# Kernel optimization log

Hardware: AMD Instinct MI355X
Metric: run time of the kernel (lower is better)

Reference implementation:

```python
import jax, jax.numpy as jnp
import numpy as np

B, TAPE, OUT, FANIN = 64, 262144, 65536, 16


def setup_inputs() -> dict:
    key = jax.random.key(0)
    k1, k2, k3, k4 = jax.random.split(key, 4)
    tape = jax.random.normal(k1, (B, TAPE), dtype=jnp.float32)
    input_indices = jax.random.randint(k2, (OUT, FANIN), 0, TAPE, dtype=jnp.int64)
    # He initialization over fanin, zeroed at padding positions (index == 0)
    weights = jax.random.normal(k3, (OUT, FANIN), dtype=jnp.float32) * np.sqrt(2.0 / FANIN)
    weights = jnp.where(input_indices == 0, 0.0, weights)
    bias = jnp.zeros((OUT,), dtype=jnp.float32)
    output_indices = jnp.arange(OUT, dtype=jnp.int64)
    act_ids = jax.random.randint(k4, (OUT,), 0, 3, dtype=jnp.int64)  # 0=relu,1=sigmoid,2=tanh
    return {"tape": tape, "weights": weights, "bias": bias,
            "input_indices": input_indices, "output_indices": output_indices,
            "act_ids": act_ids}


def reference(tape, weights, bias, input_indices, output_indices, act_ids):
    # Gather neighbor values: [B, OUT, FANIN]
    gathered = jnp.take(tape, input_indices, axis=1)
    # Weighted sum over fanin + bias: [B, OUT]
    x = jnp.einsum('bof,of->bo', gathered, weights) + bias
    # Per-node activation dispatch (vectorized select over activation groups)
    x = jnp.where(act_ids == 0, jax.nn.relu(x),
                  jnp.where(act_ids == 1, jax.nn.sigmoid(x), jnp.tanh(x)))
    # Scatter results back into the tape
    tape = tape.at[:, output_indices].set(x)
    return tape
```

## Files before the change

kernel.cpp:

```cpp
#include <hip/hip_runtime.h>
#include <hip/hip_fp16.h>

#define B_SZ 64
#define TAPE_N 262144
#define OUT_N 65536
#define FANIN 16
#define XCDS 8

typedef _Float16 h16v __attribute__((ext_vector_type(16)));
typedef _Float16 h8v  __attribute__((ext_vector_type(8)));
typedef float    f4v  __attribute__((ext_vector_type(4)));

__global__ __launch_bounds__(256) void copy_transpose_kernel(
    const float* __restrict__ tape, float* __restrict__ out,
    _Float16* __restrict__ tape_T)
{
    __shared__ float lds[64][65];
    const int t0  = blockIdx.x * 64;
    const int tid = threadIdx.x;
    const bool do_copy = (t0 >= OUT_N);

    const int t4 = tid & 15;
    const int b0 = tid >> 4;
    #pragma unroll
    for (int r = 0; r < 4; ++r) {
        const int b = b0 + r * 16;
        const f4v v = __builtin_nontemporal_load(
            (const f4v*)(tape + (size_t)b * TAPE_N + t0 + t4 * 4));
        if (do_copy)
            __builtin_nontemporal_store(
                v, (f4v*)(out + (size_t)b * TAPE_N + t0 + t4 * 4));
        lds[t4 * 4 + 0][b] = v.x;
        lds[t4 * 4 + 1][b] = v.y;
        lds[t4 * 4 + 2][b] = v.z;
        lds[t4 * 4 + 3][b] = v.w;
    }
    __syncthreads();

    const int c    = tid & 7;
    const int trow = tid >> 3;
    #pragma unroll
    for (int p = 0; p < 2; ++p) {
        const int t = trow + p * 32;
        h8v v;
        #pragma unroll
        for (int j = 0; j < 8; ++j) v[j] = (_Float16)lds[t][c * 8 + j];
        *(h8v*)(tape_T + (size_t)(t0 + t) * 64 + c * 8) = v;
    }
}

__global__ __launch_bounds__(256) void neuron_t_kernel(
    const _Float16* __restrict__ tape_T,
    const float* __restrict__ weights,
    const float* __restrict__ bias,
    const int*   __restrict__ input_indices,
    const int*   __restrict__ output_indices,
    const int*   __restrict__ act_ids,
    float* __restrict__ out)
{
    __shared__ float so[64][65];
    __shared__ int   s_ok;

    const int tid = threadIdx.x;
    const int ol  = tid >> 2;
    const int o   = blockIdx.x * 64 + ol;
    const int bq  = tid & 3;

    if (tid == 0) s_ok = 1;

    const int4*   ip = (const int4*)(input_indices + (size_t)o * FANIN);
    const float4* wp = (const float4*)(weights      + (size_t)o * FANIN);
    const int4   I0 = ip[0], I1 = ip[1], I2 = ip[2], I3 = ip[3];
    const float4 W0 = wp[0], W1 = wp[1], W2 = wp[2], W3 = wp[3];
    const float bs  = bias[o];
    const int   act = act_ids[o];
    const int   od  = output_indices[o];

    const int   idx[16] = {I0.x, I0.y, I0.z, I0.w, I1.x, I1.y, I1.z, I1.w,
                           I2.x, I2.y, I2.z, I2.w, I3.x, I3.y, I3.z, I3.w};
    const float wv[16]  = {W0.x, W0.y, W0.z, W0.w, W1.x, W1.y, W1.z, W1.w,
                           W2.x, W2.y, W2.z, W2.w, W3.x, W3.y, W3.z, W3.w};

    float acc[16];
    #pragma unroll
    for (int k = 0; k < 16; ++k) acc[k] = bs;

    const _Float16* tb = tape_T + bq * 16;

    #pragma unroll
    for (int f = 0; f < FANIN; ++f) {
        const h16v v = *(const h16v*)(tb + (size_t)idx[f] * 64);
        const float w = wv[f];
        #pragma unroll
        for (int k = 0; k < 16; ++k) acc[k] += w * (float)v[k];
    }

    if (od != o) s_ok = 0;

    #pragma unroll
    for (int k = 0; k < 16; ++k) {
        const float x = acc[k];
        float z = (act == 1) ? 0.5f * x : x;
        z = fminf(fmaxf(z, -15.0f), 15.0f);
        const float e  = __expf(-2.0f * z);
        const float th = (1.0f - e) / (1.0f + e);
        const float y = (act == 0) ? fmaxf(x, 0.0f)
                       : (act == 1) ? 0.5f * (th + 1.0f)
                                    : th;
        so[bq * 16 + k][ol] = y;
    }
    __syncthreads();

    if (s_ok) {
        const int c4 = tid & 15;
        const int rb = tid >> 4;
        const int o0 = blockIdx.x * 64;
        #pragma unroll
        for (int p = 0; p < 4; ++p) {
            const int r = rb + p * 16;
            f4v v;
            v.x = so[r][c4 * 4 + 0];
            v.y = so[r][c4 * 4 + 1];
            v.z = so[r][c4 * 4 + 2];
            v.w = so[r][c4 * 4 + 3];
            __builtin_nontemporal_store(
                v, (f4v*)(out + (size_t)r * TAPE_N + o0 + c4 * 4));
        }
    } else {
        #pragma unroll
        for (int k = 0; k < 16; ++k)
            __builtin_nontemporal_store(
                so[bq * 16 + k][ol],
                out + (size_t)(bq * 16 + k) * TAPE_N + od);
    }
}

__global__ __launch_bounds__(256) void copy_tape_kernel(
    const float4* __restrict__ src, float4* __restrict__ dst, int n4)
{
    int i = blockIdx.x * blockDim.x + threadIdx.x;
    const int stride = gridDim.x * blockDim.x;
    for (; i < n4; i += stride) dst[i] = src[i];
}

__global__ __launch_bounds__(256) void neuron_kernel(
    const float* __restrict__ tape,
    const float* __restrict__ weights,
    const float* __restrict__ bias,
    const int*   __restrict__ input_indices,
    const int*   __restrict__ output_indices,
    const int*   __restrict__ act_ids,
    float* __restrict__ out)
{
    const int grp = blockIdx.x & (XCDS - 1);
    const int j   = blockIdx.x >> 3;
    const int o   = j * 256 + threadIdx.x;

    const int4*   ip = (const int4*)(input_indices + (size_t)o * FANIN);
    const float4* wp = (const float4*)(weights      + (size_t)o * FANIN);
    const int4   i0 = ip[0], i1 = ip[1], i2 = ip[2], i3 = ip[3];
    const float4 w0 = wp[0], w1 = wp[1], w2 = wp[2], w3 = wp[3];
    const float bs  = bias[o];
    const int   act = act_ids[o];
    const int   od  = output_indices[o];

    const int b0 = grp * 8;
    #pragma unroll 1
    for (int r = 0; r < 8; ++r) {
        const int b = b0 + r;
        const float* __restrict__ t = tape + (size_t)b * TAPE_N;
        float g0  = t[i0.x], g1  = t[i0.y], g2  = t[i0.z], g3  = t[i0.w];
        float g4  = t[i1.x], g5  = t[i1.y], g6  = t[i1.z], g7  = t[i1.w];
        float g8  = t[i2.x], g9  = t[i2.y], g10 = t[i2.z], g11 = t[i2.w];
        float g12 = t[i3.x], g13 = t[i3.y], g14 = t[i3.z], g15 = t[i3.w];

        float acc = bs;
        acc += g0*w0.x;  acc += g1*w0.y;  acc += g2*w0.z;  acc += g3*w0.w;
        acc += g4*w1.x;  acc += g5*w1.y;  acc += g6*w1.z;  acc += g7*w1.w;
        acc += g8*w2.x;  acc += g9*w2.y;  acc += g10*w2.z; acc += g11*w2.w;
        acc += g12*w3.x; acc += g13*w3.y; acc += g14*w3.z; acc += g15*w3.w;

        const float x = acc;
        float z = (act == 1) ? 0.5f * x : x;
        z = fminf(fmaxf(z, -15.0f), 15.0f);
        const float e  = __expf(-2.0f * z);
        const float th = (1.0f - e) / (1.0f + e);
        const float y = (act == 0) ? fmaxf(x, 0.0f)
                       : (act == 1) ? 0.5f * (th + 1.0f)
                                    : th;

        out[(size_t)b * TAPE_N + od] = y;
    }
}

extern "C" void kernel_launch(void* const* d_in, const int* in_sizes, int n_in,
                              void* d_out, int out_size, void* d_ws, size_t ws_size,
                              hipStream_t stream)
{
    const float* tape           = (const float*)d_in[0];
    const float* weights        = (const float*)d_in[1];
    const float* bias           = (const float*)d_in[2];
    const int*   input_indices  = (const int*)d_in[3];
    const int*   output_indices = (const int*)d_in[4];
    const int*   act_ids        = (const int*)d_in[5];
    float*       out            = (float*)d_out;

    const size_t need = (size_t)TAPE_N * B_SZ * sizeof(_Float16);

    if (ws_size >= need) {
        _Float16* tape_T = (_Float16*)d_ws;
        copy_transpose_kernel<<<TAPE_N / 64, 256, 0, stream>>>(tape, out, tape_T);
        neuron_t_kernel<<<OUT_N / 64, 256, 0, stream>>>(
            tape_T, weights, bias, input_indices, output_indices, act_ids, out);
    } else {
        const int n4 = (B_SZ * TAPE_N) / 4;
        copy_tape_kernel<<<4096, 256, 0, stream>>>(
            (const float4*)tape, (float4*)out, n4);
        neuron_kernel<<<XCDS * (OUT_N / 256), 256, 0, stream>>>(
            tape, weights, bias, input_indices, output_indices, act_ids, out);
    }
}
```

Before: 157.7 us.

## Move tape passthrough copy from transpose kernel into neuron kernel as interleaved blocks

The transpose kernel stops writing the untouched tape region to the output. That copy now runs inside the second kernel as separate copy-role blocks, interleaved in groups of eight with the neuron blocks. The goal is to make the streaming copy overlap the latency-bound gather work and shorten the first kernel. In exchange the copy reads the tape a second time from memory, and the neuron kernel's grid grows to 2048 blocks.

```diff
diff --git a/kernel.cpp b/kernel.cpp
--- a/kernel.cpp
+++ b/kernel.cpp
@@ -11,14 +11,12 @@
 typedef _Float16 h8v  __attribute__((ext_vector_type(8)));
 typedef float    f4v  __attribute__((ext_vector_type(4)));
 
-__global__ __launch_bounds__(256) void copy_transpose_kernel(
-    const float* __restrict__ tape, float* __restrict__ out,
-    _Float16* __restrict__ tape_T)
+__global__ __launch_bounds__(256) void transpose_kernel(
+    const float* __restrict__ tape, _Float16* __restrict__ tape_T)
 {
     __shared__ float lds[64][65];
     const int t0  = blockIdx.x * 64;
     const int tid = threadIdx.x;
-    const bool do_copy = (t0 >= OUT_N);
 
     const int t4 = tid & 15;
     const int b0 = tid >> 4;
@@ -27,9 +25,6 @@
         const int b = b0 + r * 16;
         const f4v v = __builtin_nontemporal_load(
             (const f4v*)(tape + (size_t)b * TAPE_N + t0 + t4 * 4));
-        if (do_copy)
-            __builtin_nontemporal_store(
-                v, (f4v*)(out + (size_t)b * TAPE_N + t0 + t4 * 4));
         lds[t4 * 4 + 0][b] = v.x;
         lds[t4 * 4 + 1][b] = v.y;
         lds[t4 * 4 + 2][b] = v.z;
@@ -49,7 +44,8 @@
     }
 }
 
-__global__ __launch_bounds__(256) void neuron_t_kernel(
+__global__ __launch_bounds__(256) void neuron_copy_kernel(
+    const float* __restrict__ tape,
     const _Float16* __restrict__ tape_T,
     const float* __restrict__ weights,
     const float* __restrict__ bias,
@@ -61,9 +57,28 @@
     __shared__ float so[64][65];
     __shared__ int   s_ok;
 
-    const int tid = threadIdx.x;
+    const int bid  = blockIdx.x;
+    const int tid  = threadIdx.x;
+    const int role = (bid >> 3) & 1;
+    const int j    = (bid >> 4) * 8 + (bid & 7);
+
+    if (role == 0) {
+        const int b   = j >> 4;
+        const int seg = j & 15;
+        const float* src = tape + (size_t)b * TAPE_N + OUT_N + seg * 12288;
+        float*       dst = out  + (size_t)b * TAPE_N + OUT_N + seg * 12288;
+        f4v v[12];
+        #pragma unroll
+        for (int s = 0; s < 12; ++s)
+            v[s] = __builtin_nontemporal_load((const f4v*)src + tid + s * 256);
+        #pragma unroll
+        for (int s = 0; s < 12; ++s)
+            __builtin_nontemporal_store(v[s], (f4v*)dst + tid + s * 256);
+        return;
+    }
+
     const int ol  = tid >> 2;
-    const int o   = blockIdx.x * 64 + ol;
+    const int o   = j * 64 + ol;
     const int bq  = tid & 3;
 
     if (tid == 0) s_ok = 1;
@@ -114,7 +129,7 @@
     if (s_ok) {
         const int c4 = tid & 15;
         const int rb = tid >> 4;
-        const int o0 = blockIdx.x * 64;
+        const int o0 = j * 64;
         #pragma unroll
         for (int p = 0; p < 4; ++p) {
             const int r = rb + p * 16;
@@ -209,9 +224,10 @@
 
     if (ws_size >= need) {
         _Float16* tape_T = (_Float16*)d_ws;
-        copy_transpose_kernel<<<TAPE_N / 64, 256, 0, stream>>>(tape, out, tape_T);
-        neuron_t_kernel<<<OUT_N / 64, 256, 0, stream>>>(
-            tape_T, weights, bias, input_indices, output_indices, act_ids, out);
+        transpose_kernel<<<TAPE_N / 64, 256, 0, stream>>>(tape, tape_T);
+        neuron_copy_kernel<<<2048, 256, 0, stream>>>(
+            tape, tape_T, weights, bias, input_indices, output_indices,
+            act_ids, out);
     } else {
         const int n4 = (B_SZ * TAPE_N) / 4;
         copy_tape_kernel<<<4096, 256, 0, stream>>>(
```

Result: no change. 160.2 us (+1.6%).
